# Kernel tuning notes

Hardware: AMD Instinct MI355X
Metric: run time of the kernel (lower is better)

## Reference

```python
import jax, jax.numpy as jnp
import numpy as np

N_NODES = 50000
N_EDGES = 800000
IN_DIM = 128
HID_DIM = 128
OUT_DIM = 128
LEAKY_SLOPE = 0.01  # torch F.leaky_relu default


def setup_inputs() -> dict:
    key = jax.random.key(0)
    ks = jax.random.split(key, 10)
    src = jax.random.randint(ks[0], (N_EDGES,), 0, N_NODES)
    dst = jax.random.randint(ks[1], (N_EDGES,), 0, N_NODES)
    x = jax.random.normal(ks[2], (N_NODES, IN_DIM), dtype=jnp.float32)
    mask = jnp.ones((HID_DIM,), dtype=jnp.float32)
    # GraphConv 1 (in -> hid), with bias (DGL default)
    W1 = jax.random.normal(ks[3], (IN_DIM, HID_DIM), dtype=jnp.float32) * (1.0 / np.sqrt(IN_DIM))
    b1 = jnp.zeros((HID_DIM,), dtype=jnp.float32)
    # BicliqueAttentionLayer (hid -> hid), linear has no bias
    Wa = jax.random.normal(ks[4], (HID_DIM, HID_DIM), dtype=jnp.float32) * (1.0 / np.sqrt(HID_DIM))
    a = jax.random.normal(ks[5], (HID_DIM, 1), dtype=jnp.float32) * (1.414 / np.sqrt(HID_DIM))
    # GraphConv 2 (hid -> out)
    W2 = jax.random.normal(ks[6], (HID_DIM, OUT_DIM), dtype=jnp.float32) * (1.0 / np.sqrt(HID_DIM))
    b2 = jnp.zeros((OUT_DIM,), dtype=jnp.float32)
    return {"src": src, "dst": dst, "x": x, "mask": mask,
            "W1": W1, "b1": b1, "Wa": Wa, "a": a, "W2": W2, "b2": b2}


def _inv_sqrt_deg(idx, n):
    deg = jax.ops.segment_sum(jnp.ones(idx.shape[0], jnp.float32), idx, num_segments=n)
    return jnp.where(deg > 0, jax.lax.rsqrt(jnp.maximum(deg, 1.0)), 0.0)


def _graph_conv(h, src, dst, W, b):
    # DGL GraphConv norm='both': D_out^{-1/2} on src side, aggregate, D_in^{-1/2} on dst side
    n = h.shape[0]
    norm_src = _inv_sqrt_deg(src, n)   # out-degree of source nodes
    norm_dst = _inv_sqrt_deg(dst, n)   # in-degree of destination nodes
    h = (h @ W) * norm_src[:, None]    # project first (same math, smaller if out<in)
    agg = jax.ops.segment_sum(h[src], dst, num_segments=n)  # scatter-sum to dst
    return agg * norm_dst[:, None] + b


def _biclique_attn(h, src, dst, mask, Wa, a):
    n = h.shape[0]
    hm = (h * mask[None, :]) @ Wa                      # [N, hid]
    score_node = jnp.squeeze(hm @ a, -1)               # [N] per-node attn logit
    score = jax.nn.leaky_relu(score_node[src], LEAKY_SLOPE)  # [E]
    # segment softmax keyed by dst
    smax = jax.ops.segment_max(score, dst, num_segments=n)   # -inf for empty segments
    e = jnp.exp(score - smax[dst])
    ssum = jax.ops.segment_sum(e, dst, num_segments=n)
    alpha = e / ssum[dst]                              # [E]
    h_new = jax.ops.segment_sum(hm[src] * alpha[:, None], dst, num_segments=n)
    return jax.nn.relu(h_new)


def reference(src, dst, x, mask, W1, b1, Wa, a, W2, b2):
    h = jax.nn.relu(_graph_conv(x, src, dst, W1, b1))
    h = _biclique_attn(h, src, dst, mask, Wa, a)
    h = jax.nn.relu(_graph_conv(h, src, dst, W2, b2))
    return h
```

## Files before the change

### kernel.cpp

```cpp
#include <hip/hip_runtime.h>
#include <hip/hip_fp16.h>
#include <math.h>

#define NNODES 50000
#define NEDGES 800000
#define DIM 128
#define NCOARSE 196
#define SCHUNK 4096
#define KPAD 136
#define BCAP 6144

static inline int ceil_div(int a, int b){ return (a + b - 1) / b; }

__device__ __forceinline__ float leaky01(float x){ return x > 0.f ? x : 0.01f * x; }

typedef _Float16 f16;
typedef f16 f16x4 __attribute__((ext_vector_type(4)));
typedef f16 f16x8 __attribute__((ext_vector_type(8)));
typedef float f32x4 __attribute__((ext_vector_type(4)));


__global__ void init_cur(int* __restrict__ dcur, int* __restrict__ scur){
    int t = threadIdx.x;
    if (t < NCOARSE){ dcur[t] = t * BCAP; scur[t] = t * BCAP; }
}

__global__ __launch_bounds__(256) void coarse_scatter(const int* __restrict__ src,
    const int* __restrict__ dst, int* __restrict__ dcur, int* __restrict__ scur,
    int* __restrict__ dbuf, unsigned char* __restrict__ sbuf, int E)
{
    __shared__ int hist[NCOARSE], loff[NCOARSE], gbase[NCOARSE], cur[NCOARSE];
    __shared__ int ws4[4];
    __shared__ int stage[SCHUNK];
    int t = threadIdx.x;
    int lane = t & 63, w = t >> 6;
    int base = blockIdx.x * SCHUNK;
    int lim = base + SCHUNK < E ? base + SCHUNK : E;
    int cnt = lim - base;

    if (t < NCOARSE) hist[t] = 0;
    __syncthreads();
    for (int i = base + t; i < lim; i += 256)
        atomicAdd(&hist[dst[i] >> 8], 1);
    __syncthreads();
    {
        int v = (t < NCOARSE) ? hist[t] : 0;
        int inc = v;
        #pragma unroll
        for (int d = 1; d < 64; d <<= 1){ int u = __shfl_up(inc, d); if (lane >= d) inc += u; }
        if (lane == 63) ws4[w] = inc;
        __syncthreads();
        if (t == 0){ int r = 0;
            #pragma unroll
            for (int k = 0; k < 4; ++k){ int xx = ws4[k]; ws4[k] = r; r += xx; } }
        __syncthreads();
        if (t < NCOARSE){
            int excl = ws4[w] + inc - v;
            loff[t] = excl; cur[t] = excl;
            gbase[t] = v ? atomicAdd(&dcur[t], v) : 0;
        }
    }
    __syncthreads();
    for (int i = base + t; i < lim; i += 256){
        int d = dst[i], s = src[i];
        int b = d >> 8;
        int pos = atomicAdd(&cur[b], 1);
        stage[pos] = (b << 24) | ((d & 255) << 16) | s;
    }
    __syncthreads();
    for (int i = t; i < cnt; i += 256){
        int v = stage[i];
        int b = (int)((unsigned)v >> 24);
        dbuf[gbase[b] + (i - loff[b])] = v;
    }
    __syncthreads();

    if (t < NCOARSE) hist[t] = 0;
    __syncthreads();
    for (int i = base + t; i < lim; i += 256)
        atomicAdd(&hist[src[i] >> 8], 1);
    __syncthreads();
    {
        int v = (t < NCOARSE) ? hist[t] : 0;
        int inc = v;
        #pragma unroll
        for (int d = 1; d < 64; d <<= 1){ int u = __shfl_up(inc, d); if (lane >= d) inc += u; }
        if (lane == 63) ws4[w] = inc;
        __syncthreads();
        if (t == 0){ int r = 0;
            #pragma unroll
            for (int k = 0; k < 4; ++k){ int xx = ws4[k]; ws4[k] = r; r += xx; } }
        __syncthreads();
        if (t < NCOARSE){
            int excl = ws4[w] + inc - v;
            loff[t] = excl; cur[t] = excl;
            gbase[t] = v ? atomicAdd(&scur[t], v) : 0;
        }
    }
    __syncthreads();
    unsigned short* st16 = (unsigned short*)stage;
    for (int i = base + t; i < lim; i += 256){
        int s = src[i];
        int b = s >> 8;
        int pos = atomicAdd(&cur[b], 1);
        st16[pos] = (unsigned short)((b << 8) | (s & 255));
    }
    __syncthreads();
    for (int i = t; i < cnt; i += 256){
        int v = st16[i];
        int b = v >> 8;
        sbuf[gbase[b] + (i - loff[b])] = (unsigned char)(v & 255);
    }
}

__global__ __launch_bounds__(256) void bucket_dst(const int* __restrict__ dbuf,
    const int* __restrict__ dcur, int* __restrict__ rbeg, int* __restrict__ rend,
    float* __restrict__ nd, unsigned short* __restrict__ csrc)
{
    int b = blockIdx.x;
    int beg = b * BCAP, end = dcur[b];
    __shared__ int h[256], off[256], cur[256];
    __shared__ int ws4[4];
    int t = threadIdx.x;
    h[t] = 0; cur[t] = 0;
    __syncthreads();
    for (int i = beg + t; i < end; i += 256)
        atomicAdd(&h[(dbuf[i] >> 16) & 255], 1);
    __syncthreads();
    int v = h[t];
    int lane = t & 63, w = t >> 6, inc = v;
    #pragma unroll
    for (int d = 1; d < 64; d <<= 1){
        int u = __shfl_up(inc, d);
        if (lane >= d) inc += u;
    }
    if (lane == 63) ws4[w] = inc;
    __syncthreads();
    if (t == 0){
        int r = 0;
        #pragma unroll
        for (int k = 0; k < 4; ++k){ int xx = ws4[k]; ws4[k] = r; r += xx; }
    }
    __syncthreads();
    off[t] = ws4[w] + inc - v;
    __syncthreads();
    int d = b * 256 + t;
    if (d < NNODES){
        rbeg[d] = beg + off[t];
        rend[d] = beg + off[t] + v;
        nd[d] = v > 0 ? rsqrtf((float)v) : 0.f;
    }
    for (int i = beg + t; i < end; i += 256){
        int pv = dbuf[i];
        int j = (pv >> 16) & 255;
        int pos = atomicAdd(&cur[j], 1);
        csrc[beg + off[j] + pos] = (unsigned short)(pv & 0xFFFF);
    }
}

__global__ __launch_bounds__(256) void bucket_src(const unsigned char* __restrict__ sbuf,
    const int* __restrict__ scur, float* __restrict__ ns)
{
    int b = blockIdx.x;
    int beg = b * BCAP, end = scur[b];
    __shared__ int h[256];
    int t = threadIdx.x;
    h[t] = 0;
    __syncthreads();
    for (int i = beg + t; i < end; i += 256)
        atomicAdd(&h[sbuf[i]], 1);
    __syncthreads();
    int s = b * 256 + t;
    if (s < NNODES) ns[s] = h[t] > 0 ? rsqrtf((float)h[t]) : 0.f;
}

__global__ void waa_kernel(const float* __restrict__ Wa, const float* __restrict__ a,
                           const float* __restrict__ mask, float* __restrict__ waam){
    int gtid = blockIdx.x * blockDim.x + threadIdx.x;
    int k = gtid >> 6, lane = threadIdx.x & 63;
    if (k >= DIM) return;
    float2 v  = *(const float2*)(Wa + (long long)k * DIM + lane * 2);
    float2 av = *(const float2*)(a + lane * 2);
    float s = fmaf(v.x, av.x, v.y * av.y);
    #pragma unroll
    for (int off = 32; off > 0; off >>= 1) s += __shfl_down(s, off);
    if (lane == 0) waam[k] = s * mask[k];
}

template<typename TIN, bool USE_MASK, bool USE_ROWSCALE>
__global__ __launch_bounds__(256) void gemm_mfma(const TIN* __restrict__ in,
    const float* __restrict__ W, const float* __restrict__ mask,
    const float* __restrict__ rowscale, __half* __restrict__ out, int n)
{
    __shared__ f16 Ws[DIM][KPAD];
    __shared__ f16 Xs[64][KPAD];
    const int t = threadIdx.x;

    #pragma unroll
    for (int i = 0; i < 16; ++i){
        int idx = i * 256 + t;
        int c = idx & 127, k0 = (idx >> 7) * 4;
        f16x4 h;
        #pragma unroll
        for (int u = 0; u < 4; ++u){
            float v = W[(long long)(k0 + u) * DIM + c];
            if (USE_MASK) v *= mask[k0 + u];
            h[u] = (f16)v;
        }
        *(f16x4*)&Ws[c][k0] = h;
    }
    const int row0 = blockIdx.x * 64;
    if constexpr (sizeof(TIN) == 4){
        #pragma unroll
        for (int i = 0; i < 8; ++i){
            int idx = i * 256 + t;
            int r = idx >> 5, c4 = (idx & 31) * 4;
            int row = row0 + r;
            float4 v = make_float4(0.f, 0.f, 0.f, 0.f);
            if (row < n) v = *(const float4*)((const float*)in + (long long)row * DIM + c4);
            f16x4 h = { (f16)v.x, (f16)v.y, (f16)v.z, (f16)v.w };
            *(f16x4*)&Xs[r][c4] = h;
        }
    } else {
        #pragma unroll
        for (int i = 0; i < 4; ++i){
            int idx = i * 256 + t;
            int r = idx >> 4, c8 = (idx & 15) * 8;
            int row = row0 + r;
            f16x8 h = { (f16)0, (f16)0, (f16)0, (f16)0, (f16)0, (f16)0, (f16)0, (f16)0 };
            if (row < n) h = *(const f16x8*)((const f16*)in + (long long)row * DIM + c8);
            *(f16x8*)&Xs[r][c8] = h;
        }
    }
    __syncthreads();

    const int lane = t & 63, wid = t >> 6;
    const int l15 = lane & 15, lg = lane >> 4;
    const int wrow = wid * 16;

    f16x8 a[4];
    #pragma unroll
    for (int kc = 0; kc < 4; ++kc)
        a[kc] = *(const f16x8*)&Xs[wrow + l15][kc * 32 + lg * 8];

    float rs[4];
    #pragma unroll
    for (int r = 0; r < 4; ++r){
        int row = row0 + wrow + lg * 4 + r;
        rs[r] = (USE_ROWSCALE && row < n) ? rowscale[row] : 1.f;
    }

    #pragma unroll
    for (int ct = 0; ct < 8; ++ct){
        f32x4 acc = {0.f, 0.f, 0.f, 0.f};
        #pragma unroll
        for (int kc = 0; kc < 4; ++kc){
            f16x8 b = *(const f16x8*)&Ws[ct * 16 + l15][kc * 32 + lg * 8];
            acc = __builtin_amdgcn_mfma_f32_16x16x32_f16(a[kc], b, acc, 0, 0, 0);
        }
        int col = ct * 16 + l15;
        #pragma unroll
        for (int r = 0; r < 4; ++r){
            int row = row0 + wrow + lg * 4 + r;
            if (row < n)
                out[(long long)row * DIM + col] = __float2half(acc[r] * rs[r]);
        }
    }
}

__device__ __forceinline__ void acc8(float* acc, uint4 u, float w){
    float2 f0 = __half22float2(*(__half2*)&u.x);
    float2 f1 = __half22float2(*(__half2*)&u.y);
    float2 f2 = __half22float2(*(__half2*)&u.z);
    float2 f3 = __half22float2(*(__half2*)&u.w);
    acc[0] = fmaf(f0.x, w, acc[0]); acc[1] = fmaf(f0.y, w, acc[1]);
    acc[2] = fmaf(f1.x, w, acc[2]); acc[3] = fmaf(f1.y, w, acc[3]);
    acc[4] = fmaf(f2.x, w, acc[4]); acc[5] = fmaf(f2.y, w, acc[5]);
    acc[6] = fmaf(f3.x, w, acc[6]); acc[7] = fmaf(f3.y, w, acc[7]);
}

template<bool SCORE, typename TOUT>
__global__ __launch_bounds__(256) void agg_conv(const int* __restrict__ rbeg,
    const int* __restrict__ rend, const unsigned short* __restrict__ csrc,
    const __half* __restrict__ p, const float* __restrict__ norm,
    const float* __restrict__ b, const float* __restrict__ waam,
    TOUT* __restrict__ out, float* __restrict__ score, int n)
{
    int wave = (blockIdx.x * blockDim.x + threadIdx.x) >> 6;
    int nwaves = (gridDim.x * blockDim.x) >> 6;
    int lane = threadIdx.x & 63;
    int g = lane >> 4, l16 = lane & 15;

    float4 b0 = *(const float4*)(b + l16 * 8);
    float4 b1 = *(const float4*)(b + l16 * 8 + 4);
    float4 w0, w1;
    if (SCORE){
        w0 = *(const float4*)(waam + l16 * 8);
        w1 = *(const float4*)(waam + l16 * 8 + 4);
    }

    for (int node = wave; node < n; node += nwaves){
        int beg = rbeg[node], end = rend[node];
        float acc[8] = {0.f, 0.f, 0.f, 0.f, 0.f, 0.f, 0.f, 0.f};
        for (int i = beg + g; i < end; i += 4){
            int s = csrc[i];
            uint4 u = *(const uint4*)(p + (long long)s * DIM + l16 * 8);
            acc8(acc, u, 1.f);
        }
        #pragma unroll
        for (int k = 0; k < 8; ++k){
            acc[k] += __shfl_xor(acc[k], 16);
            acc[k] += __shfl_xor(acc[k], 32);
        }
        float nd = norm[node];
        float o[8];
        o[0] = fmaxf(fmaf(acc[0], nd, b0.x), 0.f);
        o[1] = fmaxf(fmaf(acc[1], nd, b0.y), 0.f);
        o[2] = fmaxf(fmaf(acc[2], nd, b0.z), 0.f);
        o[3] = fmaxf(fmaf(acc[3], nd, b0.w), 0.f);
        o[4] = fmaxf(fmaf(acc[4], nd, b1.x), 0.f);
        o[5] = fmaxf(fmaf(acc[5], nd, b1.y), 0.f);
        o[6] = fmaxf(fmaf(acc[6], nd, b1.z), 0.f);
        o[7] = fmaxf(fmaf(acc[7], nd, b1.w), 0.f);
        if (g == 0){
            if constexpr (sizeof(TOUT) == 2){
                __half2 h0 = __floats2half2_rn(o[0], o[1]);
                __half2 h1 = __floats2half2_rn(o[2], o[3]);
                __half2 h2 = __floats2half2_rn(o[4], o[5]);
                __half2 h3 = __floats2half2_rn(o[6], o[7]);
                uint4 u;
                u.x = *(unsigned*)&h0; u.y = *(unsigned*)&h1;
                u.z = *(unsigned*)&h2; u.w = *(unsigned*)&h3;
                *(uint4*)((__half*)out + (long long)node * DIM + l16 * 8) = u;
            } else {
                float* orow = (float*)out + (long long)node * DIM + l16 * 8;
                *(float4*)(orow)     = make_float4(o[0], o[1], o[2], o[3]);
                *(float4*)(orow + 4) = make_float4(o[4], o[5], o[6], o[7]);
            }
        }
        if (SCORE){
            float sc = o[0]*w0.x + o[1]*w0.y + o[2]*w0.z + o[3]*w0.w
                     + o[4]*w1.x + o[5]*w1.y + o[6]*w1.z + o[7]*w1.w;
            #pragma unroll
            for (int d = 1; d < 16; d <<= 1) sc += __shfl_xor(sc, d);
            if (lane == 0) score[node] = sc;
        }
    }
}

__global__ __launch_bounds__(256) void agg_attn(const int* __restrict__ rbeg,
    const int* __restrict__ rend, const unsigned short* __restrict__ csrc,
    const __half* __restrict__ hm, const float* __restrict__ score,
    __half* __restrict__ out, int n)
{
    int wave = (blockIdx.x * blockDim.x + threadIdx.x) >> 6;
    int nwaves = (gridDim.x * blockDim.x) >> 6;
    int lane = threadIdx.x & 63;
    int g = lane >> 4, l16 = lane & 15;

    for (int node = wave; node < n; node += nwaves){
        int beg = rbeg[node], end = rend[node];

        int i0 = beg + lane;
        int s_l = 0; float v_l = -1e30f;
        if (i0 < end){ s_l = csrc[i0]; v_l = leaky01(score[s_l]); }

        float m = v_l;
        for (int i = i0 + 64; i < end; i += 64) m = fmaxf(m, leaky01(score[csrc[i]]));
        #pragma unroll
        for (int off = 32; off > 0; off >>= 1) m = fmaxf(m, __shfl_xor(m, off));

        float w_l = (i0 < end) ? __expf(v_l - m) : 0.f;
        float ss = w_l;
        for (int i = i0 + 64; i < end; i += 64) ss += __expf(leaky01(score[csrc[i]]) - m);
        #pragma unroll
        for (int off = 32; off > 0; off >>= 1) ss += __shfl_xor(ss, off);
        float inv = ss > 0.f ? 1.f / ss : 0.f;

        float acc[8] = {0.f, 0.f, 0.f, 0.f, 0.f, 0.f, 0.f, 0.f};
        {
            int cl = end - beg; if (cl > 64) cl = 64;
            for (int j4 = 0; j4 < cl; j4 += 4){
                int j = j4 + g;
                int jj = j < cl ? j : 0;
                float w = __shfl(w_l, jj);
                int s = __shfl(s_l, jj);
                if (j < cl){
                    uint4 u = *(const uint4*)(hm + (long long)s * DIM + l16 * 8);
                    acc8(acc, u, w);
                }
            }
        }
        for (int cb = beg + 64; cb < end; cb += 64){
            int cl = end - cb; if (cl > 64) cl = 64;
            int s2 = 0; float w2 = 0.f;
            if (lane < cl){
                s2 = csrc[cb + lane];
                w2 = __expf(leaky01(score[s2]) - m);
            }
            for (int j4 = 0; j4 < cl; j4 += 4){
                int j = j4 + g;
                int jj = j < cl ? j : 0;
                float w = __shfl(w2, jj);
                int s = __shfl(s2, jj);
                if (j < cl){
                    uint4 u = *(const uint4*)(hm + (long long)s * DIM + l16 * 8);
                    acc8(acc, u, w);
                }
            }
        }
        #pragma unroll
        for (int k = 0; k < 8; ++k){
            acc[k] += __shfl_xor(acc[k], 16);
            acc[k] += __shfl_xor(acc[k], 32);
        }
        if (g == 0){
            float o[8];
            #pragma unroll
            for (int k = 0; k < 8; ++k) o[k] = fmaxf(acc[k] * inv, 0.f);
            __half2 h0 = __floats2half2_rn(o[0], o[1]);
            __half2 h1 = __floats2half2_rn(o[2], o[3]);
            __half2 h2 = __floats2half2_rn(o[4], o[5]);
            __half2 h3 = __floats2half2_rn(o[6], o[7]);
            uint4 u;
            u.x = *(unsigned*)&h0; u.y = *(unsigned*)&h1;
            u.z = *(unsigned*)&h2; u.w = *(unsigned*)&h3;
            *(uint4*)(out + (long long)node * DIM + l16 * 8) = u;
        }
    }
}


extern "C" void kernel_launch(void* const* d_in, const int* in_sizes, int n_in,
                              void* d_out, int out_size, void* d_ws, size_t ws_size,
                              hipStream_t stream)
{
    const int*   src  = (const int*)d_in[0];
    const int*   dst  = (const int*)d_in[1];
    const float* x    = (const float*)d_in[2];
    const float* mask = (const float*)d_in[3];
    const float* W1   = (const float*)d_in[4];
    const float* b1   = (const float*)d_in[5];
    const float* Wa   = (const float*)d_in[6];
    const float* a    = (const float*)d_in[7];
    const float* W2   = (const float*)d_in[8];
    const float* b2   = (const float*)d_in[9];
    float* out = (float*)d_out;

    const int N = NNODES, E = NEDGES;
    const long long NB = (long long)N * DIM;
    const long long BSLOTS = (long long)NCOARSE * BCAP;

    __half* bufH     = (__half*)d_ws;
    __half* bufH2    = bufH + NB;
    float*  norm_src = (float*)(bufH2 + NB);
    float*  norm_dst = norm_src + N;
    float*  score    = norm_dst + N;
    float*  waam     = score + N;
    int*    dcur     = (int*)(waam + DIM);
    int*    scur     = dcur + NCOARSE;
    int*    rbeg     = scur + NCOARSE;
    int*    rend     = rbeg + N;
    int*    dbuf     = rend + N;
    unsigned short* csrc = (unsigned short*)(dbuf + BSLOTS);
    unsigned char*  sbuf = (unsigned char*)(csrc + BSLOTS);

    init_cur<<<1, 256, 0, stream>>>(dcur, scur);
    coarse_scatter<<<ceil_div(E, SCHUNK), 256, 0, stream>>>(src, dst, dcur, scur, dbuf, sbuf, E);
    bucket_dst<<<NCOARSE, 256, 0, stream>>>(dbuf, dcur, rbeg, rend, norm_dst, csrc);
    bucket_src<<<NCOARSE, 256, 0, stream>>>(sbuf, scur, norm_src);
    waa_kernel<<<ceil_div(DIM * 64, 256), 256, 0, stream>>>(Wa, a, mask, waam);

    gemm_mfma<float, false, true><<<ceil_div(N, 64), 256, 0, stream>>>(x, W1, nullptr, norm_src, bufH, N);
    agg_conv<true, __half><<<2048, 256, 0, stream>>>(rbeg, rend, csrc, bufH, norm_dst, b1, waam, bufH2, score, N);

    gemm_mfma<__half, true, false><<<ceil_div(N, 64), 256, 0, stream>>>(bufH2, Wa, mask, nullptr, bufH, N);
    agg_attn<<<2048, 256, 0, stream>>>(rbeg, rend, csrc, bufH, score, bufH2, N);

    gemm_mfma<__half, false, true><<<ceil_div(N, 64), 256, 0, stream>>>(bufH2, W2, nullptr, norm_src, bufH, N);
    agg_conv<false, float><<<2048, 256, 0, stream>>>(rbeg, rend, csrc, bufH, norm_dst, b2, nullptr, out, nullptr, N);
}
```

Baseline: 208.9 us.

## Merge preprocessing launches, stage bucket data in LDS, unroll gather loops

```diff
diff --git a/kernel.cpp b/kernel.cpp
--- a/kernel.cpp
+++ b/kernel.cpp
@@ -6,7 +6,7 @@
 #define NEDGES 800000
 #define DIM 128
 #define NCOARSE 196
-#define SCHUNK 4096
+#define SCHUNK 2048
 #define KPAD 136
 #define BCAP 6144
 
@@ -19,10 +19,19 @@
 typedef f16 f16x8 __attribute__((ext_vector_type(8)));
 typedef float f32x4 __attribute__((ext_vector_type(4)));
 
-
-__global__ void init_cur(int* __restrict__ dcur, int* __restrict__ scur){
-    int t = threadIdx.x;
-    if (t < NCOARSE){ dcur[t] = t * BCAP; scur[t] = t * BCAP; }
+__global__ void waa_init(const float* __restrict__ Wa, const float* __restrict__ a,
+                         const float* __restrict__ mask, float* __restrict__ waam,
+                         int* __restrict__ dcur, int* __restrict__ scur){
+    int gtid = blockIdx.x * blockDim.x + threadIdx.x;
+    if (gtid < NCOARSE){ dcur[gtid] = gtid * BCAP; scur[gtid] = gtid * BCAP; }
+    int k = gtid >> 6, lane = threadIdx.x & 63;
+    if (k >= DIM) return;
+    float2 v  = *(const float2*)(Wa + (long long)k * DIM + lane * 2);
+    float2 av = *(const float2*)(a + lane * 2);
+    float s = fmaf(v.x, av.x, v.y * av.y);
+    #pragma unroll
+    for (int off = 32; off > 0; off >>= 1) s += __shfl_down(s, off);
+    if (lane == 0) waam[k] = s * mask[k];
 }
 
 __global__ __launch_bounds__(256) void coarse_scatter(const int* __restrict__ src,
@@ -113,78 +122,67 @@
     }
 }
 
-__global__ __launch_bounds__(256) void bucket_dst(const int* __restrict__ dbuf,
-    const int* __restrict__ dcur, int* __restrict__ rbeg, int* __restrict__ rend,
-    float* __restrict__ nd, unsigned short* __restrict__ csrc)
-{
-    int b = blockIdx.x;
-    int beg = b * BCAP, end = dcur[b];
+__global__ __launch_bounds__(256) void bucket_all(const int* __restrict__ dbuf,
+    const unsigned char* __restrict__ sbuf, const int* __restrict__ dcur,
+    const int* __restrict__ scur, int* __restrict__ rbeg, int* __restrict__ rend,
+    float* __restrict__ nd, float* __restrict__ ns, unsigned short* __restrict__ csrc)
+{
+    __shared__ int stage[BCAP];
     __shared__ int h[256], off[256], cur[256];
     __shared__ int ws4[4];
     int t = threadIdx.x;
-    h[t] = 0; cur[t] = 0;
-    __syncthreads();
-    for (int i = beg + t; i < end; i += 256)
-        atomicAdd(&h[(dbuf[i] >> 16) & 255], 1);
-    __syncthreads();
-    int v = h[t];
-    int lane = t & 63, w = t >> 6, inc = v;
-    #pragma unroll
-    for (int d = 1; d < 64; d <<= 1){
-        int u = __shfl_up(inc, d);
-        if (lane >= d) inc += u;
-    }
-    if (lane == 63) ws4[w] = inc;
-    __syncthreads();
-    if (t == 0){
-        int r = 0;
-        #pragma unroll
-        for (int k = 0; k < 4; ++k){ int xx = ws4[k]; ws4[k] = r; r += xx; }
-    }
-    __syncthreads();
-    off[t] = ws4[w] + inc - v;
-    __syncthreads();
-    int d = b * 256 + t;
-    if (d < NNODES){
-        rbeg[d] = beg + off[t];
-        rend[d] = beg + off[t] + v;
-        nd[d] = v > 0 ? rsqrtf((float)v) : 0.f;
-    }
-    for (int i = beg + t; i < end; i += 256){
-        int pv = dbuf[i];
-        int j = (pv >> 16) & 255;
-        int pos = atomicAdd(&cur[j], 1);
-        csrc[beg + off[j] + pos] = (unsigned short)(pv & 0xFFFF);
-    }
-}
-
-__global__ __launch_bounds__(256) void bucket_src(const unsigned char* __restrict__ sbuf,
-    const int* __restrict__ scur, float* __restrict__ ns)
-{
     int b = blockIdx.x;
-    int beg = b * BCAP, end = scur[b];
-    __shared__ int h[256];
-    int t = threadIdx.x;
-    h[t] = 0;
-    __syncthreads();
-    for (int i = beg + t; i < end; i += 256)
-        atomicAdd(&h[sbuf[i]], 1);
-    __syncthreads();
-    int s = b * 256 + t;
-    if (s < NNODES) ns[s] = h[t] > 0 ? rsqrtf((float)h[t]) : 0.f;
-}
-
-__global__ void waa_kernel(const float* __restrict__ Wa, const float* __restrict__ a,
-                           const float* __restrict__ mask, float* __restrict__ waam){
-    int gtid = blockIdx.x * blockDim.x + threadIdx.x;
-    int k = gtid >> 6, lane = threadIdx.x & 63;
-    if (k >= DIM) return;
-    float2 v  = *(const float2*)(Wa + (long long)k * DIM + lane * 2);
-    float2 av = *(const float2*)(a + lane * 2);
-    float s = fmaf(v.x, av.x, v.y * av.y);
-    #pragma unroll
-    for (int off = 32; off > 0; off >>= 1) s += __shfl_down(s, off);
-    if (lane == 0) waam[k] = s * mask[k];
+
+    if (b < NCOARSE){
+        int beg = b * BCAP, end = dcur[b], cnt = end - beg;
+        h[t] = 0; cur[t] = 0;
+        __syncthreads();
+        for (int i = t; i < cnt; i += 256){
+            int v = dbuf[beg + i];
+            stage[i] = v;
+            atomicAdd(&h[(v >> 16) & 255], 1);
+        }
+        __syncthreads();
+        int v = h[t];
+        int lane = t & 63, w = t >> 6, inc = v;
+        #pragma unroll
+        for (int d = 1; d < 64; d <<= 1){
+            int u = __shfl_up(inc, d);
+            if (lane >= d) inc += u;
+        }
+        if (lane == 63) ws4[w] = inc;
+        __syncthreads();
+        if (t == 0){
+            int r = 0;
+            #pragma unroll
+            for (int k = 0; k < 4; ++k){ int xx = ws4[k]; ws4[k] = r; r += xx; }
+        }
+        __syncthreads();
+        off[t] = ws4[w] + inc - v;
+        __syncthreads();
+        int d = b * 256 + t;
+        if (d < NNODES){
+            rbeg[d] = beg + off[t];
+            rend[d] = beg + off[t] + v;
+            nd[d] = v > 0 ? rsqrtf((float)v) : 0.f;
+        }
+        for (int i = t; i < cnt; i += 256){
+            int pv = stage[i];
+            int j = (pv >> 16) & 255;
+            int pos = atomicAdd(&cur[j], 1);
+            csrc[beg + off[j] + pos] = (unsigned short)(pv & 0xFFFF);
+        }
+    } else {
+        b -= NCOARSE;
+        int beg = b * BCAP, end = scur[b];
+        h[t] = 0;
+        __syncthreads();
+        for (int i = beg + t; i < end; i += 256)
+            atomicAdd(&h[sbuf[i]], 1);
+        __syncthreads();
+        int s = b * 256 + t;
+        if (s < NNODES) ns[s] = h[t] > 0 ? rsqrtf((float)h[t]) : 0.f;
+    }
 }
 
 template<typename TIN, bool USE_MASK, bool USE_ROWSCALE>
@@ -302,7 +300,15 @@
     for (int node = wave; node < n; node += nwaves){
         int beg = rbeg[node], end = rend[node];
         float acc[8] = {0.f, 0.f, 0.f, 0.f, 0.f, 0.f, 0.f, 0.f};
-        for (int i = beg + g; i < end; i += 4){
+        int i = beg + g;
+        for (; i + 5 <= end; i += 8){
+            int s0 = csrc[i], s1 = csrc[i + 4];
+            uint4 u0 = *(const uint4*)(p + (long long)s0 * DIM + l16 * 8);
+            uint4 u1 = *(const uint4*)(p + (long long)s1 * DIM + l16 * 8);
+            acc8(acc, u0, 1.f);
+            acc8(acc, u1, 1.f);
+        }
+        for (; i < end; i += 4){
             int s = csrc[i];
             uint4 u = *(const uint4*)(p + (long long)s * DIM + l16 * 8);
             acc8(acc, u, 1.f);
@@ -380,7 +386,17 @@
         float acc[8] = {0.f, 0.f, 0.f, 0.f, 0.f, 0.f, 0.f, 0.f};
         {
             int cl = end - beg; if (cl > 64) cl = 64;
-            for (int j4 = 0; j4 < cl; j4 += 4){
+            int j4 = 0;
+            for (; j4 + 8 <= cl; j4 += 8){
+                int jA = j4 + g, jB = j4 + 4 + g;
+                float wA = __shfl(w_l, jA), wB = __shfl(w_l, jB);
+                int sA = __shfl(s_l, jA), sB = __shfl(s_l, jB);
+                uint4 uA = *(const uint4*)(hm + (long long)sA * DIM + l16 * 8);
+                uint4 uB = *(const uint4*)(hm + (long long)sB * DIM + l16 * 8);
+                acc8(acc, uA, wA);
+                acc8(acc, uB, wB);
+            }
+            for (; j4 < cl; j4 += 4){
                 int j = j4 + g;
                 int jj = j < cl ? j : 0;
                 float w = __shfl(w_l, jj);
@@ -465,11 +481,10 @@
     unsigned short* csrc = (unsigned short*)(dbuf + BSLOTS);
     unsigned char*  sbuf = (unsigned char*)(csrc + BSLOTS);
 
-    init_cur<<<1, 256, 0, stream>>>(dcur, scur);
+    waa_init<<<ceil_div(DIM * 64, 256), 256, 0, stream>>>(Wa, a, mask, waam, dcur, scur);
     coarse_scatter<<<ceil_div(E, SCHUNK), 256, 0, stream>>>(src, dst, dcur, scur, dbuf, sbuf, E);
-    bucket_dst<<<NCOARSE, 256, 0, stream>>>(dbuf, dcur, rbeg, rend, norm_dst, csrc);
-    bucket_src<<<NCOARSE, 256, 0, stream>>>(sbuf, scur, norm_src);
-    waa_kernel<<<ceil_div(DIM * 64, 256), 256, 0, stream>>>(Wa, a, mask, waam);
+    bucket_all<<<2 * NCOARSE, 256, 0, stream>>>(dbuf, sbuf, dcur, scur, rbeg, rend,
+                                                norm_dst, norm_src, csrc);
 
     gemm_mfma<float, false, true><<<ceil_div(N, 64), 256, 0, stream>>>(x, W1, nullptr, norm_src, bufH, N);
     agg_conv<true, __half><<<2048, 256, 0, stream>>>(rbeg, rend, csrc, bufH, norm_dst, b1, waam, bufH2, score, N);
```

New measurement: 192.9 us. -7.7%, faster.
